# Performance work log

Measured on AMD Instinct MI355X. Metric: run time of the kernel, lower is better.

Reference implementation:

```python
import jax, jax.numpy as jnp
import numpy as np
import math

PATCH = 41
NUM_ANG = 8
NUM_SPATIAL = 4
BIN_KSIZE = 2 * int(PATCH / (NUM_SPATIAL + 1))   # 16
BIN_STRIDE = PATCH // NUM_SPATIAL                # 10
BIN_PAD = BIN_KSIZE // 4                         # 4
CLIPVAL = 0.2
EPS = 1e-10
N = 8192


def _sift_pooling_kernel(ksize: int) -> np.ndarray:
    k2 = float(ksize) / 2.0
    xc2 = k2 - np.abs(np.arange(ksize, dtype=np.float32) + 0.5 - k2)
    return (np.outer(xc2, xc2) / k2 ** 2).astype(np.float32)


def _sift_weighting_kernel(ksize: int) -> np.ndarray:
    # Gauss, vlfeat sigma: sigma_mul_2 = ksize**2
    k2 = float(ksize) / 2.0
    ys = np.arange(ksize, dtype=np.float32)[:, None]
    xs = np.arange(ksize, dtype=np.float32)[None, :]
    disq = (ys - k2 + 0.5) ** 2 + (xs - k2 + 0.5) ** 2
    return np.exp(-disq / float(ksize ** 2)).astype(np.float32)


def setup_inputs() -> dict:
    key = jax.random.key(0)
    x = jax.random.normal(key, (N, 1, PATCH, PATCH), dtype=jnp.float32)
    gk = jnp.asarray(_sift_weighting_kernel(PATCH))   # [41,41]
    pk = jnp.asarray(_sift_pooling_kernel(BIN_KSIZE))  # [16,16]
    return {"x": x, "gk": gk, "pk": pk}


def _l2_normalize(v):
    return v / jnp.maximum(jnp.linalg.norm(v, axis=1, keepdims=True), 1e-12)


def reference(x, gk, pk):
    # gradients via replicate-pad + central difference (matches [-1,0,1] convs)
    xp = jnp.pad(x, ((0, 0), (0, 0), (0, 0), (1, 1)), mode='edge')
    gx = xp[..., 2:] - xp[..., :-2]
    yp = jnp.pad(x, ((0, 0), (0, 0), (1, 1), (0, 0)), mode='edge')
    gy = yp[:, :, 2:, :] - yp[:, :, :-2, :]

    mag = jnp.sqrt(gx * gx + gy * gy + EPS) * gk  # gaussian-weighted magnitude
    ori = jnp.arctan2(gy, gx + EPS)

    # soft angular binning
    o_big = (ori + 2.0 * math.pi) / (2.0 * math.pi) * NUM_ANG
    bo0f = jnp.floor(o_big)
    wo1 = o_big - bo0f
    bo0 = bo0f.astype(jnp.int32) % NUM_ANG
    bo1 = (bo0 + 1) % NUM_ANG
    # [N,1,P,P,nb]
    contrib = (jax.nn.one_hot(bo0, NUM_ANG, dtype=mag.dtype) * ((1.0 - wo1) * mag)[..., None]
               + jax.nn.one_hot(bo1, NUM_ANG, dtype=mag.dtype) * (wo1 * mag)[..., None])
    contrib = jnp.transpose(contrib[:, 0], (0, 3, 1, 2))  # [N,nb,P,P]

    # depthwise weighted spatial pooling (same triangular kernel per angular bin)
    kern = jnp.broadcast_to(pk[None, None], (NUM_ANG, 1, BIN_KSIZE, BIN_KSIZE))
    pooled = jax.lax.conv_general_dilated(
        contrib, kern,
        window_strides=(BIN_STRIDE, BIN_STRIDE),
        padding=[(BIN_PAD, BIN_PAD), (BIN_PAD, BIN_PAD)],
        feature_group_count=NUM_ANG,
        dimension_numbers=('NCHW', 'OIHW', 'NCHW'))  # [N,nb,4,4]

    desc = pooled.reshape(pooled.shape[0], -1)  # [N,128]
    desc = _l2_normalize(desc)
    desc = jnp.clip(desc, 0.0, CLIPVAL)
    desc = _l2_normalize(desc)
    # rootsift: sqrt of L1-normalized descriptor
    desc = desc / jnp.maximum(jnp.sum(jnp.abs(desc), axis=1, keepdims=True), 1e-12)
    return jnp.sqrt(desc + 1e-10)
```

## Files before the change

kernel.cpp:

```cpp
#include <hip/hip_runtime.h>
#include <hip/hip_fp16.h>
#include <math.h>

#define PATCH 41
#define PP 1681
#define NB 8
#define STRIDE 10
#define PAD 4
#define NTH 256
#define CPIX (PP + 14)

__device__ __forceinline__ constexpr float tri16(int k) {
    float d = (float)k + 0.5f - 8.0f;
    float a = d < 0.0f ? -d : d;
    return (8.0f - a) * 0.125f;
}

__device__ __forceinline__ float block_sum(float v, float* s_red, int t) {
    #pragma unroll
    for (int o = 32; o > 0; o >>= 1) v += __shfl_xor(v, o);
    if ((t & 63) == 0) s_red[t >> 6] = v;
    __syncthreads();
    float total = s_red[0] + s_red[1] + s_red[2] + s_red[3];
    __syncthreads();
    return total;
}

__global__ __launch_bounds__(NTH, 5) void sift_desc_kernel(
        const float* __restrict__ x,
        const float* __restrict__ gk,
        const float* __restrict__ pk,
        float* __restrict__ out)
{
    const int patch = blockIdx.x;
    const int t = threadIdx.x;

    __shared__ __align__(16) __half s_c[CPIX * NB];
    __shared__ __align__(16) char s_xbuf[(PP + 7) * 2];
    __shared__ float s_red[4];
    __half* s_x = (__half*)s_xbuf;
    __half* s_H = (__half*)s_xbuf;

    const float* xp = x + (size_t)patch * PP;
    for (int p = t; p < PP; p += NTH) s_x[p] = __float2half(xp[p]);
    if (t < 14) {
        uint4 z; z.x = z.y = z.z = z.w = 0u;
        int idx = (t < 4) ? t : (PP + t);
        *(uint4*)&s_c[idx * NB] = z;
    }
    __syncthreads();

    for (int p = t; p < PP; p += NTH) {
        int i = p / PATCH;
        int j = p - i * PATCH;
        float xl = __half2float(s_x[p - (j > 0)]);
        float xr = __half2float(s_x[p + (j < PATCH - 1)]);
        float xu = __half2float(s_x[p - (i > 0) * PATCH]);
        float xd = __half2float(s_x[p + (i < PATCH - 1) * PATCH]);
        float gxv = xr - xl;
        float gyv = xd - xu;
        float X = gxv + 1e-10f;

        float di = (float)(i - 20), dj = (float)(j - 20);
        float gkv = __builtin_amdgcn_exp2f((di * di + dj * dj) * -8.582362e-4f);
        float mag = __builtin_amdgcn_sqrtf(fmaf(gxv, gxv, fmaf(gyv, gyv, 1e-10f))) * gkv;

        float ax = fabsf(X), ay = fabsf(gyv);
        float mx = fmaxf(ax, ay), mn = fminf(ax, ay);
        float r = mn * __builtin_amdgcn_rcpf(fmaxf(mx, 1e-30f));
        float r2 = r * r;
        float a4 = fmaf(r2, -0.0149238f, 0.0670406f);
        a4 = fmaf(r2, a4, -0.1482457f);
        a4 = fmaf(r2, a4, 0.2464287f);
        a4 = fmaf(r2, a4, -0.4235106f);
        a4 = fmaf(r2, a4, 1.2732106f);
        a4 *= r;

        bool sw = ay > ax;
        bool xn = X < 0.0f;
        bool yn = gyv < 0.0f;
        int q = (xn ? 2 : 0) + ((sw != xn) ? 1 : 0);
        int b0 = yn ? 7 - q : q;
        bool f = (sw != xn) != yn;
        float ma = a4 * mag;
        float mb = mag - ma;
        float v0 = f ? ma : mb;
        float v1 = f ? mb : ma;

        unsigned v0h = (unsigned)__half_as_ushort(__float2half(v0));
        unsigned v1h = (unsigned)__half_as_ushort(__float2half(v1));
        bool odd = (b0 & 1) != 0;
        unsigned wA = odd ? (v0h << 16) : (v0h | (v1h << 16));
        unsigned wB = odd ? v1h : 0u;
        int rA = b0 >> 1;
        int rB = (rA + 1) & 3;
        uint4 cw;
        cw.x = (rA == 0 ? wA : 0u) | (rB == 0 ? wB : 0u);
        cw.y = (rA == 1 ? wA : 0u) | (rB == 1 ? wB : 0u);
        cw.z = (rA == 2 ? wA : 0u) | (rB == 2 ? wB : 0u);
        cw.w = (rA == 3 ? wA : 0u) | (rB == 3 ? wB : 0u);
        *(uint4*)&s_c[(p + 4) * NB] = cw;
    }
    __syncthreads();

    if (t < PATCH * 4) {
        const int row = t >> 2;
        const int ox = t & 3;
        const int sbase = row * PATCH + ox * STRIDE;
        const __half2 z2 = __float2half2_rn(0.0f);
        __half2 a0 = z2, a1 = z2, a2 = z2, a3 = z2;
        #pragma unroll
        for (int kx = 0; kx < 16; ++kx) {
            const float w = tri16(kx);
            __half2 wp = __float2half2_rn(w);
            if (kx < PAD)  wp = (ox > 0) ? wp : z2;
            if (kx == 15)  wp = (ox < 3) ? wp : z2;
            uint4 cwv = *(const uint4*)&s_c[(sbase + kx) * NB];
            a0 = __hfma2(wp, *(__half2*)&cwv.x, a0);
            a1 = __hfma2(wp, *(__half2*)&cwv.y, a1);
            a2 = __hfma2(wp, *(__half2*)&cwv.z, a2);
            a3 = __hfma2(wp, *(__half2*)&cwv.w, a3);
        }
        uint4 hv;
        hv.x = *(unsigned*)&a0;
        hv.y = *(unsigned*)&a1;
        hv.z = *(unsigned*)&a2;
        hv.w = *(unsigned*)&a3;
        *(uint4*)&s_H[(row * 4 + ox) * NB] = hv;
    }
    __syncthreads();

    float v = 0.0f;
    if (t < 128) {
        int b = t >> 4;
        int oy = (t >> 2) & 3;
        int ox = t & 3;
        #pragma unroll
        for (int ky = 0; ky < 16; ++ky) {
            const float w = tri16(ky);
            int iy = oy * STRIDE - PAD + ky;
            int iyc = min(max(iy, 0), PATCH - 1);
            float hv = __half2float(s_H[(iyc * 4 + ox) * NB + b]);
            v = fmaf((iy == iyc) ? w : 0.0f, hv, v);
        }
    }

    float sumsq = block_sum(v * v, s_red, t);
    v *= 1.0f / fmaxf(__builtin_amdgcn_sqrtf(sumsq), 1e-12f);
    v = fminf(fmaxf(v, 0.0f), 0.2f);

    float sumsq2 = block_sum(v * v, s_red, t);
    v *= 1.0f / fmaxf(__builtin_amdgcn_sqrtf(sumsq2), 1e-12f);

    float l1 = block_sum(v, s_red, t);
    v = v / fmaxf(l1, 1e-12f);

    if (t < 128) out[(size_t)patch * 128 + t] = __builtin_amdgcn_sqrtf(v + 1e-10f);
}

extern "C" void kernel_launch(void* const* d_in, const int* in_sizes, int n_in,
                              void* d_out, int out_size, void* d_ws, size_t ws_size,
                              hipStream_t stream) {
    const float* x  = (const float*)d_in[0];
    const float* gk = (const float*)d_in[1];
    const float* pk = (const float*)d_in[2];
    float* out = (float*)d_out;
    const int n = in_sizes[0] / PP;
    sift_desc_kernel<<<n, NTH, 0, stream>>>(x, gk, pk, out);
}
```

Before: 124.7 us.

## Register-tile gradient stage and do descriptor normalization in a single wavefront

Stores the input patch with edge-replicated padded rows so each thread handles a 2x4 pixel strip and slides three row registers to reuse loads for the central differences. The per-pixel Gaussian exp is precomputed as a separable row/column table, and the contribution packing uses cvt_pkrtz with 64-bit shifts. The three block-wide reductions, each with two barriers, are replaced by one barrier and shuffle reductions inside a single 64-lane wavefront handling two values per lane. Only 231 threads are active in the gradient stage, and more unrolled code may raise register pressure.

```diff
diff --git a/kernel.cpp b/kernel.cpp
--- a/kernel.cpp
+++ b/kernel.cpp
@@ -9,6 +9,8 @@
 #define PAD 4
 #define NTH 256
 #define CPIX (PP + 14)
+#define XROW 44
+#define XSZ (PATCH * XROW)
 
 __device__ __forceinline__ constexpr float tri16(int k) {
     float d = (float)k + 0.5f - 8.0f;
@@ -16,14 +18,51 @@
     return (8.0f - a) * 0.125f;
 }
 
-__device__ __forceinline__ float block_sum(float v, float* s_red, int t) {
-    #pragma unroll
-    for (int o = 32; o > 0; o >>= 1) v += __shfl_xor(v, o);
-    if ((t & 63) == 0) s_red[t >> 6] = v;
-    __syncthreads();
-    float total = s_red[0] + s_red[1] + s_red[2] + s_red[3];
-    __syncthreads();
-    return total;
+__device__ __forceinline__ void load4(const __half* s, int k,
+                                      float& f0, float& f1, float& f2, float& f3) {
+    __half2 lo = *(const __half2*)&s[k];
+    __half2 hi = *(const __half2*)&s[k + 2];
+    f0 = __low2float(lo);  f1 = __high2float(lo);
+    f2 = __low2float(hi);  f3 = __high2float(hi);
+}
+
+__device__ __forceinline__ uint4 pixel_contrib(float gx, float gy, float gauss) {
+    float X = gx + 1e-10f;
+    float mag = __builtin_amdgcn_sqrtf(fmaf(gx, gx, fmaf(gy, gy, 1e-10f))) * gauss;
+
+    float ax = fabsf(X), ay = fabsf(gy);
+    float mx = fmaxf(ax, ay), mn = fminf(ax, ay);
+    float r = mn * __builtin_amdgcn_rcpf(fmaxf(mx, 1e-30f));
+    float r2 = r * r;
+    float a4 = fmaf(r2, -0.0149238f, 0.0670406f);
+    a4 = fmaf(r2, a4, -0.1482457f);
+    a4 = fmaf(r2, a4, 0.2464287f);
+    a4 = fmaf(r2, a4, -0.4235106f);
+    a4 = fmaf(r2, a4, 1.2732106f);
+    a4 *= r;
+
+    bool sw = ay > ax;
+    bool xn = X < 0.0f;
+    bool yn = gy < 0.0f;
+    int q = (xn ? 2 : 0) + ((sw != xn) ? 1 : 0);
+    int b0 = yn ? 7 - q : q;
+    bool f = (sw != xn) != yn;
+    float ma = a4 * mag;
+    float mb = mag - ma;
+    float v0 = f ? ma : mb;
+    float v1 = f ? mb : ma;
+
+    unsigned combo = __builtin_bit_cast(unsigned, __builtin_amdgcn_cvt_pkrtz(v0, v1));
+    int sh = (b0 & 3) << 4;
+    unsigned long long A = (unsigned long long)combo << sh;
+    unsigned long long B = ((b0 & 3) == 3) ? (unsigned long long)(combo >> 16) : 0ull;
+    bool lohalf = b0 < 4;
+    unsigned long long lo = lohalf ? A : B;
+    unsigned long long hi = lohalf ? B : A;
+    uint4 cw;
+    cw.x = (unsigned)lo; cw.y = (unsigned)(lo >> 32);
+    cw.z = (unsigned)hi; cw.w = (unsigned)(hi >> 32);
+    return cw;
 }
 
 __global__ __launch_bounds__(NTH, 5) void sift_desc_kernel(
@@ -36,13 +75,22 @@
     const int t = threadIdx.x;
 
     __shared__ __align__(16) __half s_c[CPIX * NB];
-    __shared__ __align__(16) char s_xbuf[(PP + 7) * 2];
-    __shared__ float s_red[4];
-    __half* s_x = (__half*)s_xbuf;
-    __half* s_H = (__half*)s_xbuf;
-
+    __shared__ __align__(16) __half s_xp[XSZ];
+    __shared__ float s_rc[PATCH];
+    __half* s_H = s_xp;
+    float* s_desc = reinterpret_cast<float*>(s_c);
+
+    if (t < PATCH) {
+        float d = (float)(t - 20);
+        s_rc[t] = __builtin_amdgcn_exp2f(d * d * -8.582362e-4f);
+    }
     const float* xp = x + (size_t)patch * PP;
-    for (int p = t; p < PP; p += NTH) s_x[p] = __float2half(xp[p]);
+    for (int idx = t; idx < XSZ; idx += NTH) {
+        int i = idx / XROW;
+        int jj = idx - i * XROW - 1;
+        int jc = min(max(jj, 0), PATCH - 1);
+        s_xp[idx] = __float2half(xp[i * PATCH + jc]);
+    }
     if (t < 14) {
         uint4 z; z.x = z.y = z.z = z.w = 0u;
         int idx = (t < 4) ? t : (PP + t);
@@ -50,56 +98,44 @@
     }
     __syncthreads();
 
-    for (int p = t; p < PP; p += NTH) {
-        int i = p / PATCH;
-        int j = p - i * PATCH;
-        float xl = __half2float(s_x[p - (j > 0)]);
-        float xr = __half2float(s_x[p + (j < PATCH - 1)]);
-        float xu = __half2float(s_x[p - (i > 0) * PATCH]);
-        float xd = __half2float(s_x[p + (i < PATCH - 1) * PATCH]);
-        float gxv = xr - xl;
-        float gyv = xd - xu;
-        float X = gxv + 1e-10f;
-
-        float di = (float)(i - 20), dj = (float)(j - 20);
-        float gkv = __builtin_amdgcn_exp2f((di * di + dj * dj) * -8.582362e-4f);
-        float mag = __builtin_amdgcn_sqrtf(fmaf(gxv, gxv, fmaf(gyv, gyv, 1e-10f))) * gkv;
-
-        float ax = fabsf(X), ay = fabsf(gyv);
-        float mx = fmaxf(ax, ay), mn = fminf(ax, ay);
-        float r = mn * __builtin_amdgcn_rcpf(fmaxf(mx, 1e-30f));
-        float r2 = r * r;
-        float a4 = fmaf(r2, -0.0149238f, 0.0670406f);
-        a4 = fmaf(r2, a4, -0.1482457f);
-        a4 = fmaf(r2, a4, 0.2464287f);
-        a4 = fmaf(r2, a4, -0.4235106f);
-        a4 = fmaf(r2, a4, 1.2732106f);
-        a4 *= r;
-
-        bool sw = ay > ax;
-        bool xn = X < 0.0f;
-        bool yn = gyv < 0.0f;
-        int q = (xn ? 2 : 0) + ((sw != xn) ? 1 : 0);
-        int b0 = yn ? 7 - q : q;
-        bool f = (sw != xn) != yn;
-        float ma = a4 * mag;
-        float mb = mag - ma;
-        float v0 = f ? ma : mb;
-        float v1 = f ? mb : ma;
-
-        unsigned v0h = (unsigned)__half_as_ushort(__float2half(v0));
-        unsigned v1h = (unsigned)__half_as_ushort(__float2half(v1));
-        bool odd = (b0 & 1) != 0;
-        unsigned wA = odd ? (v0h << 16) : (v0h | (v1h << 16));
-        unsigned wB = odd ? v1h : 0u;
-        int rA = b0 >> 1;
-        int rB = (rA + 1) & 3;
-        uint4 cw;
-        cw.x = (rA == 0 ? wA : 0u) | (rB == 0 ? wB : 0u);
-        cw.y = (rA == 1 ? wA : 0u) | (rB == 1 ? wB : 0u);
-        cw.z = (rA == 2 ? wA : 0u) | (rB == 2 ? wB : 0u);
-        cw.w = (rA == 3 ? wA : 0u) | (rB == 3 ? wB : 0u);
-        *(uint4*)&s_c[(p + 4) * NB] = cw;
+    if (t < 231) {
+        const int strip = t / 21;
+        const int pairc = t - strip * 21;
+        const int j = 2 * pairc;
+        const int i0 = 4 * strip;
+        const float cf0 = s_rc[j];
+        const float cf1 = s_rc[min(j + 1, PATCH - 1)];
+        const bool has1 = (j < PATCH - 1);
+
+        const int kMax = (PATCH - 1) * XROW + j;
+        int kA = max(i0 - 1, 0) * XROW + j;
+        int kB = i0 * XROW + j;
+        float A0, A1, A2, A3, B0, B1, B2, B3;
+        load4(s_xp, kA, A0, A1, A2, A3);
+        load4(s_xp, kB, B0, B1, B2, B3);
+        int kC = min(kB + XROW, kMax);
+        int pbase = (i0 * PATCH + j + 4) * NB;
+
+        #pragma unroll
+        for (int r = 0; r < 4; ++r) {
+            const int i = i0 + r;
+            const bool ok = (i < PATCH);
+            float C0, C1, C2, C3;
+            load4(s_xp, kC, C0, C1, C2, C3);
+            float rf = s_rc[min(i, PATCH - 1)];
+
+            uint4 cw0 = pixel_contrib(B2 - B0, C1 - A1, rf * cf0);
+            uint4 cw1 = pixel_contrib(B3 - B1, C2 - A2, rf * cf1);
+            if (ok) {
+                *(uint4*)&s_c[pbase] = cw0;
+                if (has1) *(uint4*)&s_c[pbase + NB] = cw1;
+            }
+
+            A0 = B0; A1 = B1; A2 = B2; A3 = B3;
+            B0 = C0; B1 = C1; B2 = C2; B3 = C3;
+            kC = min(kC + XROW, kMax);
+            pbase += PATCH * NB;
+        }
     }
     __syncthreads();
 
@@ -143,19 +179,36 @@
             float hv = __half2float(s_H[(iyc * 4 + ox) * NB + b]);
             v = fmaf((iy == iyc) ? w : 0.0f, hv, v);
         }
-    }
-
-    float sumsq = block_sum(v * v, s_red, t);
-    v *= 1.0f / fmaxf(__builtin_amdgcn_sqrtf(sumsq), 1e-12f);
-    v = fminf(fmaxf(v, 0.0f), 0.2f);
-
-    float sumsq2 = block_sum(v * v, s_red, t);
-    v *= 1.0f / fmaxf(__builtin_amdgcn_sqrtf(sumsq2), 1e-12f);
-
-    float l1 = block_sum(v, s_red, t);
-    v = v / fmaxf(l1, 1e-12f);
-
-    if (t < 128) out[(size_t)patch * 128 + t] = __builtin_amdgcn_sqrtf(v + 1e-10f);
+        s_desc[t] = v;
+    }
+    __syncthreads();
+
+    if (t < 64) {
+        float a = s_desc[t];
+        float b = s_desc[t + 64];
+
+        float ss = fmaf(a, a, b * b);
+        #pragma unroll
+        for (int o = 32; o > 0; o >>= 1) ss += __shfl_xor(ss, o);
+        float inv = 1.0f / fmaxf(__builtin_amdgcn_sqrtf(ss), 1e-12f);
+        a = fminf(fmaxf(a * inv, 0.0f), 0.2f);
+        b = fminf(fmaxf(b * inv, 0.0f), 0.2f);
+
+        float ss2 = fmaf(a, a, b * b);
+        #pragma unroll
+        for (int o = 32; o > 0; o >>= 1) ss2 += __shfl_xor(ss2, o);
+        float inv2 = 1.0f / fmaxf(__builtin_amdgcn_sqrtf(ss2), 1e-12f);
+        a *= inv2; b *= inv2;
+
+        float l1 = a + b;
+        #pragma unroll
+        for (int o = 32; o > 0; o >>= 1) l1 += __shfl_xor(l1, o);
+        float invl = 1.0f / fmaxf(l1, 1e-12f);
+
+        float* op = out + (size_t)patch * 128;
+        op[t]      = __builtin_amdgcn_sqrtf(fmaf(a, invl, 1e-10f));
+        op[t + 64] = __builtin_amdgcn_sqrtf(fmaf(b, invl, 1e-10f));
+    }
 }
 
 extern "C" void kernel_launch(void* const* d_in, const int* in_sizes, int n_in,
```

Result: no change. 123.3 us (-1.0%).
